# Kernel tuning notes

Hardware: AMD Instinct MI355X
Metric: run time of the kernel (lower is better)

Reference implementation:

```python
import jax, jax.numpy as jnp
import numpy as np

N = 8192
DX = 1.0 / 8192.0
N_MODES = 12


def setup_inputs() -> dict:
    key = jax.random.key(0)
    k1, k2, k3 = jax.random.split(key, 3)
    return {
        "a0": jax.random.normal(k1, (1,), dtype=jnp.float32),
        "cos_coeff": jax.random.normal(k2, (N_MODES,), dtype=jnp.float32),
        "sin_coeff": jax.random.normal(k3, (N_MODES,), dtype=jnp.float32),
    }


def _lowfreq_potential(a0, cos_coeff, sin_coeff):
    # x in [0, 1] with N points (matches torch.linspace)
    x = jnp.linspace(0.0, 1.0, N, dtype=jnp.float32)  # [N]
    k = jnp.arange(1, N_MODES + 1, dtype=jnp.float32)  # [M]
    phase = 2.0 * jnp.pi * k[:, None] * x[None, :]      # [M, N]
    V = a0 + cos_coeff @ jnp.cos(phase) + sin_coeff @ jnp.sin(phase)  # [N]
    return V


def reference(a0, cos_coeff, sin_coeff):
    inv_dx2 = jnp.float32(1.0 / DX**2)
    # Tridiagonal Laplacian: 2 on diag, -1 on off-diagonals, scaled by 1/dx^2
    L = (2.0 * jnp.eye(N, dtype=jnp.float32)
         - jnp.eye(N, k=1, dtype=jnp.float32)
         - jnp.eye(N, k=-1, dtype=jnp.float32)) * inv_dx2
    V = _lowfreq_potential(a0, cos_coeff, sin_coeff)  # [N]
    H = L + jnp.diag(V)
    H = 0.5 * (H + H.T)
    return jnp.nan_to_num(H, nan=0.0, posinf=0.0, neginf=0.0)
```

## Files before the change

kernel.cpp:

```cpp
#include <hip/hip_runtime.h>
#include <math.h>

#define N 8192
#define N_MODES 12


__global__ __launch_bounds__(256) void schro_band_only_kernel(
    const float* __restrict__ a0,
    const float* __restrict__ cos_c,
    const float* __restrict__ sin_c,
    float* __restrict__ out)
{
    const int row = blockIdx.x * blockDim.x + threadIdx.x;
    if (row >= N) return;

    const float inv_dx2 = 67108864.0f;

    const float x = (float)row * (1.0f / (float)(N - 1));
    float V = a0[0];
    #pragma unroll
    for (int k = 0; k < N_MODES; ++k) {
        const float ph = 6.28318530717958647692f * (float)(k + 1) * x;
        V += cos_c[k] * cosf(ph) + sin_c[k] * sinf(ph);
    }

    float* o = out + (long long)row * N;
    o[row] = 2.0f * inv_dx2 + V;
    if (row > 0)     o[row - 1] = -inv_dx2;
    if (row < N - 1) o[row + 1] = -inv_dx2;
}

extern "C" void kernel_launch(void* const* d_in, const int* in_sizes, int n_in,
                              void* d_out, int out_size, void* d_ws, size_t ws_size,
                              hipStream_t stream) {
    const float* a0    = (const float*)d_in[0];
    const float* cos_c = (const float*)d_in[1];
    const float* sin_c = (const float*)d_in[2];
    float* out = (float*)d_out;

    hipMemsetAsync(out, 0, (size_t)out_size * sizeof(float), stream);

    schro_band_only_kernel<<<N / 256, 256, 0, stream>>>(a0, cos_c, sin_c, out);
}
```

Measured before the change: 254.8 us.

## Fuse zero-fill and band writes into one grid-stride float4 kernel

Replaces the separate hipMemsetAsync and the band-only kernel with a single grid-stride kernel. Each thread writes one float4 of the 256 MB output, either zeros or band values, and computes the potential V only for quads that touch the tridiagonal band. This removes one launch and the scattered, uncoalesced band writes, at the cost of relying on a hand-written store loop to match the write bandwidth of the runtime memset.

Result: slower. 269.9 us (+5.9%).

```diff
diff --git a/kernel.cpp b/kernel.cpp
--- a/kernel.cpp
+++ b/kernel.cpp
@@ -5,29 +5,48 @@
 #define N_MODES 12
 
 
-__global__ __launch_bounds__(256) void schro_band_only_kernel(
+__global__ __launch_bounds__(256) void schro_fused_fill(
     const float* __restrict__ a0,
     const float* __restrict__ cos_c,
     const float* __restrict__ sin_c,
     float* __restrict__ out)
 {
-    const int row = blockIdx.x * blockDim.x + threadIdx.x;
-    if (row >= N) return;
-
     const float inv_dx2 = 67108864.0f;
 
-    const float x = (float)row * (1.0f / (float)(N - 1));
-    float V = a0[0];
-    #pragma unroll
-    for (int k = 0; k < N_MODES; ++k) {
-        const float ph = 6.28318530717958647692f * (float)(k + 1) * x;
-        V += cos_c[k] * cosf(ph) + sin_c[k] * sinf(ph);
+    const int total_q = (N / 4) * N;
+    const int stride  = gridDim.x * blockDim.x;
+
+    float4* __restrict__ o4 = (float4*)out;
+
+    for (int q = blockIdx.x * blockDim.x + threadIdx.x; q < total_q; q += stride) {
+        const int e   = q << 2;
+        const int row = e >> 13;
+        const int c   = e & (N - 1);
+
+        float4 v = make_float4(0.0f, 0.0f, 0.0f, 0.0f);
+
+        const int d = row - c;
+        if (d >= -1 && d <= 4) {
+            const float x = (float)row * (1.0f / (float)(N - 1));
+            float V = a0[0];
+            #pragma unroll
+            for (int k = 0; k < N_MODES; ++k) {
+                const float ph = 6.28318530717958647692f * (float)(k + 1) * x;
+                V += cos_c[k] * cosf(ph) + sin_c[k] * sinf(ph);
+            }
+            const float diagv = 2.0f * inv_dx2 + V;
+
+            float* pv = &v.x;
+            #pragma unroll
+            for (int k = 0; k < 4; ++k) {
+                const int col = c + k;
+                if (col == row)                          pv[k] = diagv;
+                else if (col == row - 1 || col == row + 1) pv[k] = -inv_dx2;
+            }
+        }
+
+        o4[q] = v;
     }
-
-    float* o = out + (long long)row * N;
-    o[row] = 2.0f * inv_dx2 + V;
-    if (row > 0)     o[row - 1] = -inv_dx2;
-    if (row < N - 1) o[row + 1] = -inv_dx2;
 }
 
 extern "C" void kernel_launch(void* const* d_in, const int* in_sizes, int n_in,
@@ -38,7 +57,5 @@
     const float* sin_c = (const float*)d_in[2];
     float* out = (float*)d_out;
 
-    hipMemsetAsync(out, 0, (size_t)out_size * sizeof(float), stream);
-
-    schro_band_only_kernel<<<N / 256, 256, 0, stream>>>(a0, cos_c, sin_c, out);
+    schro_fused_fill<<<2048, 256, 0, stream>>>(a0, cos_c, sin_c, out);
 }
```

## Fuse zero fill and band writes into one nontemporal vectorized store kernel

Applied to the files above, without the earlier changes.

Replaces the separate memset plus sparse band-writing kernel with a single grid-stride kernel that writes every float4 of the 256 MB output exactly once. Each thread computes the potential only when its 4-column chunk touches the tridiagonal band, and otherwise stores zeros. Stores use nontemporal hints to avoid cache pollution. This removes one launch and the scattered second pass over the band, but now depends on the custom store loop matching memset bandwidth.

Measured after the change: 283.2 us. +11.2%, slower.

```diff
diff --git a/kernel.cpp b/kernel.cpp
--- a/kernel.cpp
+++ b/kernel.cpp
@@ -3,31 +3,52 @@
 
 #define N 8192
 #define N_MODES 12
+#define GRID 2048
+#define BLK 256
 
 
-__global__ __launch_bounds__(256) void schro_band_only_kernel(
+typedef float floatx4 __attribute__((ext_vector_type(4)));
+
+__global__ __launch_bounds__(BLK) void schro_fused_fill_nt(
     const float* __restrict__ a0,
     const float* __restrict__ cos_c,
     const float* __restrict__ sin_c,
     float* __restrict__ out)
 {
-    const int row = blockIdx.x * blockDim.x + threadIdx.x;
-    if (row >= N) return;
-
     const float inv_dx2 = 67108864.0f;
 
-    const float x = (float)row * (1.0f / (float)(N - 1));
-    float V = a0[0];
-    #pragma unroll
-    for (int k = 0; k < N_MODES; ++k) {
-        const float ph = 6.28318530717958647692f * (float)(k + 1) * x;
-        V += cos_c[k] * cosf(ph) + sin_c[k] * sinf(ph);
+    const int q0  = blockIdx.x * BLK + threadIdx.x;
+    const int c   = (q0 << 2) & (N - 1);
+    int row       = q0 >> 11;
+
+    floatx4* __restrict__ p = (floatx4*)out + q0;
+
+    #pragma unroll 1
+    for (int it = 0; it < 32; ++it) {
+        floatx4 v = (floatx4)(0.0f);
+
+        if ((unsigned)(row - c + 1) <= 5u) {
+            const float x = (float)row * (1.0f / (float)(N - 1));
+            float V = a0[0];
+            #pragma unroll
+            for (int k = 0; k < N_MODES; ++k) {
+                const float ph = 6.28318530717958647692f * (float)(k + 1) * x;
+                V += cos_c[k] * cosf(ph) + sin_c[k] * sinf(ph);
+            }
+            const float diagv = 2.0f * inv_dx2 + V;
+
+            #pragma unroll
+            for (int j = 0; j < 4; ++j) {
+                const int col = c + j;
+                if (col == row)                            v[j] = diagv;
+                else if (col == row - 1 || col == row + 1) v[j] = -inv_dx2;
+            }
+        }
+
+        __builtin_nontemporal_store(v, p);
+        p   += GRID * BLK;
+        row += 256;
     }
-
-    float* o = out + (long long)row * N;
-    o[row] = 2.0f * inv_dx2 + V;
-    if (row > 0)     o[row - 1] = -inv_dx2;
-    if (row < N - 1) o[row + 1] = -inv_dx2;
 }
 
 extern "C" void kernel_launch(void* const* d_in, const int* in_sizes, int n_in,
@@ -38,7 +59,5 @@
     const float* sin_c = (const float*)d_in[2];
     float* out = (float*)d_out;
 
-    hipMemsetAsync(out, 0, (size_t)out_size * sizeof(float), stream);
-
-    schro_band_only_kernel<<<N / 256, 256, 0, stream>>>(a0, cos_c, sin_c, out);
+    schro_fused_fill_nt<<<GRID, BLK, 0, stream>>>(a0, cos_c, sin_c, out);
 }
```

## Fuse output zeroing into the band kernel with vectorized float4 stores

Applied to the files above, without the earlier changes.

Drops the separate hipMemsetAsync. Each block of 256 threads now zeroes four full rows of the matrix with float4 stores. After a block barrier, the first four threads write the diagonal and off-diagonal values for those rows, with the potential V precomputed into shared memory. This removes one launch and lets a custom wide-store loop produce the 256 MB of zeros instead of the runtime memset. The trade-off is that store throughput now depends on this kernel's grid shape and store pattern rather than the runtime's tuned fill.

Result: no change. 255.4 us (+0.2%).

```diff
diff --git a/kernel.cpp b/kernel.cpp
--- a/kernel.cpp
+++ b/kernel.cpp
@@ -3,31 +3,54 @@
 
 #define N 8192
 #define N_MODES 12
+#define BLK 256
+#define ROWS_PER_BLOCK 4
+#define GRID (N / ROWS_PER_BLOCK)
 
 
-__global__ __launch_bounds__(256) void schro_band_only_kernel(
+typedef float floatx4 __attribute__((ext_vector_type(4)));
+
+__global__ __launch_bounds__(BLK) void schro_fill_band(
     const float* __restrict__ a0,
     const float* __restrict__ cos_c,
     const float* __restrict__ sin_c,
     float* __restrict__ out)
 {
-    const int row = blockIdx.x * blockDim.x + threadIdx.x;
-    if (row >= N) return;
+    const float inv_dx2 = 67108864.0f;
+    __shared__ float Vsh[ROWS_PER_BLOCK];
 
-    const float inv_dx2 = 67108864.0f;
+    const int b = blockIdx.x;
+    const int t = threadIdx.x;
 
-    const float x = (float)row * (1.0f / (float)(N - 1));
-    float V = a0[0];
-    #pragma unroll
-    for (int k = 0; k < N_MODES; ++k) {
-        const float ph = 6.28318530717958647692f * (float)(k + 1) * x;
-        V += cos_c[k] * cosf(ph) + sin_c[k] * sinf(ph);
+    if (t < ROWS_PER_BLOCK) {
+        const int row = b * ROWS_PER_BLOCK + t;
+        const float x = (float)row * (1.0f / (float)(N - 1));
+        float V = a0[0];
+        #pragma unroll
+        for (int k = 0; k < N_MODES; ++k) {
+            const float ph = 6.28318530717958647692f * (float)(k + 1) * x;
+            V += cos_c[k] * cosf(ph) + sin_c[k] * sinf(ph);
+        }
+        Vsh[t] = V;
     }
 
-    float* o = out + (long long)row * N;
-    o[row] = 2.0f * inv_dx2 + V;
-    if (row > 0)     o[row - 1] = -inv_dx2;
-    if (row < N - 1) o[row + 1] = -inv_dx2;
+    floatx4* __restrict__ p =
+        (floatx4*)out + (size_t)b * (ROWS_PER_BLOCK * (N / 4)) + t;
+    const floatx4 z = (floatx4)(0.0f);
+    #pragma unroll
+    for (int it = 0; it < 32; ++it) {
+        p[(size_t)it * BLK] = z;
+    }
+
+    __syncthreads();
+
+    if (t < ROWS_PER_BLOCK) {
+        const int row = b * ROWS_PER_BLOCK + t;
+        float* o = out + (size_t)row * N;
+        o[row] = 2.0f * inv_dx2 + Vsh[t];
+        if (row > 0)     o[row - 1] = -inv_dx2;
+        if (row < N - 1) o[row + 1] = -inv_dx2;
+    }
 }
 
 extern "C" void kernel_launch(void* const* d_in, const int* in_sizes, int n_in,
@@ -38,7 +61,5 @@
     const float* sin_c = (const float*)d_in[2];
     float* out = (float*)d_out;
 
-    hipMemsetAsync(out, 0, (size_t)out_size * sizeof(float), stream);
-
-    schro_band_only_kernel<<<N / 256, 256, 0, stream>>>(a0, cos_c, sin_c, out);
+    schro_fill_band<<<GRID, BLK, 0, stream>>>(a0, cos_c, sin_c, out);
 }
```
